# Performance work log

Hardware: AMD Instinct MI355X
Metric: run time of the kernel (lower is better)

## Reference

```python
import jax, jax.numpy as jnp
import numpy as np

N_NODES = 100000
N_EDGES = 1200000
N_GRAPHS = 2048
NUM_SHAPE, NUM_COLOR, NUM_CLASS = 8, 8, 10
MAX_POS, EMB, HID = 20, 16, 64
IN_DIM = 3 * EMB  # 48


def setup_inputs() -> dict:
    key = jax.random.key(0)
    ks = jax.random.split(key, 14)
    x = jax.random.randint(ks[0], (N_NODES, 3), 0, NUM_SHAPE)
    edge_index = jax.random.randint(ks[1], (2, N_EDGES), 0, N_NODES)
    batch = jnp.sort(jax.random.randint(ks[2], (N_NODES,), 0, N_GRAPHS))
    s = 0.1
    return {
        'x': x, 'edge_index': edge_index, 'batch': batch, 'num_graphs': N_GRAPHS,
        'shape_emb': jax.random.normal(ks[3], (NUM_SHAPE, EMB)) * s,
        'color_emb': jax.random.normal(ks[4], (NUM_COLOR, EMB)) * s,
        'pos_emb': jax.random.normal(ks[5], (MAX_POS, EMB)) * s,
        'W1_l': jax.random.normal(ks[6], (IN_DIM, HID)) * s,
        'W1_r': jax.random.normal(ks[7], (IN_DIM, HID)) * s,
        'b1': jnp.zeros((HID,)),
        'W2_l': jax.random.normal(ks[8], (HID, HID)) * s,
        'W2_r': jax.random.normal(ks[9], (HID, HID)) * s,
        'b2': jnp.zeros((HID,)),
        'Wc': jax.random.normal(ks[10], (HID, NUM_CLASS)) * s,
        'bc': jnp.zeros((NUM_CLASS,)),
    }


def _sage(h, src, dst, W_l, W_r, b, n_nodes):
    # mean-aggregate neighbor features x[src] into dst, then linear combine with root
    agg = jax.ops.segment_sum(h[src], dst, num_segments=n_nodes)
    deg = jax.ops.segment_sum(jnp.ones((src.shape[0],), h.dtype), dst, num_segments=n_nodes)
    mean = agg / jnp.maximum(deg, 1.0)[:, None]
    return mean @ W_l + h @ W_r + b


def reference(x, edge_index, batch, num_graphs, shape_emb, color_emb, pos_emb,
              W1_l, W1_r, b1, W2_l, W2_r, b2, Wc, bc):
    n_nodes = x.shape[0]
    shp = shape_emb[x[:, 0]]
    col = color_emb[x[:, 1]]
    pos = pos_emb[jnp.clip(x[:, 2], 0, MAX_POS - 1)]
    h = jnp.concatenate([shp, col, pos], axis=-1)  # [N, 48]
    src, dst = edge_index[0], edge_index[1]
    h = jax.nn.relu(_sage(h, src, dst, W1_l, W1_r, b1, n_nodes))
    h = jax.nn.relu(_sage(h, src, dst, W2_l, W2_r, b2, n_nodes))
    # global mean pool per graph
    gsum = jax.ops.segment_sum(h, batch, num_segments=num_graphs)
    gcnt = jax.ops.segment_sum(jnp.ones((n_nodes,), h.dtype), batch, num_segments=num_graphs)
    hg = gsum / jnp.maximum(gcnt, 1.0)[:, None]
    return hg @ Wc + bc
```

## Files before the change

kernel.cpp:

```cpp
#include <hip/hip_runtime.h>

#define N_NODES 100000
#define N_EDGES 1200000
#define N_GRAPHS 2048
#define CAPA 16
#define CAPB 32
#define NBUCK 500
#define DPB 200
#define BCAP 4864
#define TILE 4096

typedef unsigned int uint;
typedef unsigned short ushort;
typedef __attribute__((ext_vector_type(8))) short short8;
typedef __attribute__((ext_vector_type(4))) float f32x4;

__device__ __forceinline__ int atomAddI(int* p, int v) {
    return __hip_atomic_fetch_add(p, v, __ATOMIC_RELAXED, __HIP_MEMORY_SCOPE_AGENT);
}
__device__ __forceinline__ int clampPos(int v) { return min(max(v, 0), 19); }
__device__ __forceinline__ uint f2bf(float f) {
    uint b = __float_as_uint(f);
    return (b + 0x7fffu + ((b >> 16) & 1u)) >> 16;
}
__device__ __forceinline__ int bucketOf(int d) {
    return (int)(((uint)((d >> 3) * 5243)) >> 17);
}

__global__ __launch_bounds__(256) void k_init(
    const int* __restrict__ x,
    const float* __restrict__ se, const float* __restrict__ ce,
    const float* __restrict__ pe,
    const float* __restrict__ W1l, const float* __restrict__ W1r,
    const float* __restrict__ b1,
    const float* __restrict__ W2l, const float* __restrict__ W2r,
    ushort* __restrict__ WLt, ushort* __restrict__ WstkT,
    int* __restrict__ gcur, int* __restrict__ xpk) {
    int t = blockIdx.x * 256 + threadIdx.x;
    if (t < 64 * 96) {
        int col = t / 96, k = t - (t / 96) * 96;
        float v = 0.f;
        if (k < 72) {
            int bkt = (k < 36) ? k : (k - 36);
            const float* erow; int f0;
            if (bkt < 8)       { erow = se + bkt * 16;        f0 = 0;  }
            else if (bkt < 16) { erow = ce + (bkt - 8) * 16;  f0 = 16; }
            else               { erow = pe + (bkt - 16) * 16; f0 = 32; }
            const float* W = (k < 36) ? W1l : W1r;
            float a = 0.f;
            #pragma unroll
            for (int f = 0; f < 16; ++f) a = fmaf(erow[f], W[(f0 + f) * 64 + col], a);
            v = a;
        } else if (k == 72) {
            v = b1[col];
        }
        WLt[t] = (ushort)f2bf(v);
    }
    if (t < 64 * 128) {
        int col = t >> 7, k = t & 127;
        float wv = (k < 64) ? W2r[k * 64 + col] : W2l[(k - 64) * 64 + col];
        WstkT[col * 128 + k] = (ushort)f2bf(wv);
    }
    if (t < NBUCK) gcur[t] = 0;
    for (int i = t; i < N_NODES; i += 256 * 256) {
        int xs = x[i * 3 + 0], xc = x[i * 3 + 1], xp = clampPos(x[i * 3 + 2]);
        xpk[i] = xs | (xc << 8) | (xp << 16);
    }
}

__global__ __launch_bounds__(256) void k_bin(const int* __restrict__ ei,
                                             int* __restrict__ gcur,
                                             int2* __restrict__ binned) {
    __shared__ int hist[NBUCK], offs[NBUCK], runc[NBUCK], gbase[NBUCK];
    __shared__ int2 stag[TILE];
    int tid = threadIdx.x;
    int tile_base = blockIdx.x * TILE;
    int tile_n = min(TILE, N_EDGES - tile_base);
    int n4 = tile_n >> 2;
    const int4* s4p = (const int4*)(ei + tile_base);
    const int4* d4p = (const int4*)(ei + N_EDGES + tile_base);

    for (int t = tid; t < NBUCK; t += 256) hist[t] = 0;
    __syncthreads();
    for (int k = tid; k < n4; k += 256) {
        int4 d4 = d4p[k];
        #pragma unroll
        for (int i = 0; i < 4; ++i) atomicAdd(&hist[bucketOf((&d4.x)[i])], 1);
    }
    __syncthreads();
    if (tid < 64) {
        int carry = 0;
        for (int c = 0; c < 8; ++c) {
            int idx = c * 64 + tid;
            int v = (idx < NBUCK) ? hist[idx] : 0;
            int orig = v;
            #pragma unroll
            for (int o = 1; o < 64; o <<= 1) {
                int u = __shfl_up(v, o);
                if (tid >= o) v += u;
            }
            if (idx < NBUCK) offs[idx] = carry + v - orig;
            carry += __shfl(v, 63);
        }
    }
    __syncthreads();
    for (int t = tid; t < NBUCK; t += 256) runc[t] = offs[t];
    __syncthreads();
    for (int k = tid; k < n4; k += 256) {
        int4 d4 = d4p[k];
        int4 s4 = s4p[k];
        #pragma unroll
        for (int i = 0; i < 4; ++i) {
            int b = bucketOf((&d4.x)[i]);
            int pos = atomicAdd(&runc[b], 1);
            stag[pos] = make_int2((&s4.x)[i], (&d4.x)[i]);
        }
    }
    __syncthreads();
    for (int t = tid; t < NBUCK; t += 256) gbase[t] = atomAddI(&gcur[t], hist[t]);
    __syncthreads();
    for (int i = tid; i < tile_n; i += 256) {
        int2 p = stag[i];
        int b = bucketOf(p.y);
        int o = gbase[b] + (i - offs[b]);
        if (o < BCAP) binned[(size_t)b * BCAP + o] = p;
    }
}

__global__ __launch_bounds__(256) void k_place(const int2* __restrict__ binned,
                                               const int* __restrict__ gcur,
                                               int* __restrict__ cursor,
                                               int* __restrict__ slabA,
                                               int* __restrict__ slabB) {
    __shared__ int lslab[DPB][CAPA + CAPB];
    __shared__ int lcur[DPB];
    int b = blockIdx.x;
    int tid = threadIdx.x;
    if (tid < DPB) lcur[tid] = 0;
    __syncthreads();
    int n = min(gcur[b], BCAP);
    const int2* in = binned + (size_t)b * BCAP;
    for (int i = tid; i < n; i += 256) {
        int2 p = in[i];
        int local = p.y - b * DPB;
        int slot = atomicAdd(&lcur[local], 1);
        if (slot < CAPA + CAPB) lslab[local][slot] = p.x;
    }
    __syncthreads();
    for (int i = tid; i < DPB * CAPA; i += 256)
        slabA[b * DPB * CAPA + i] = lslab[i >> 4][i & 15];
    for (int i = tid; i < DPB * CAPB; i += 256)
        slabB[b * DPB * CAPB + i] = lslab[i >> 5][CAPA + (i & 31)];
    if (tid < DPB) cursor[b * DPB + tid] = lcur[tid];
}

__device__ __forceinline__ int slabAt(const int* __restrict__ slabA,
                                      const int* __restrict__ slabB,
                                      int row, int idx) {
    return (idx < CAPA) ? slabA[row * CAPA + idx] : slabB[row * CAPB + idx - CAPA];
}

__global__ __launch_bounds__(256) void k_layer1(
    const int* __restrict__ xpk, const int* __restrict__ cursor,
    const int* __restrict__ slabA, const int* __restrict__ slabB,
    const ushort* __restrict__ WLt, uint* __restrict__ AbU) {
    __shared__ int    cnt[16][104];
    __shared__ ushort scnt[16][104];
    __shared__ float  sinv[16];
    __shared__ int    sdeg[16];
    int tid = threadIdx.x;
    int row0 = blockIdx.x * 16;
    for (int i = tid; i < 16 * 104; i += 256) cnt[i / 104][i % 104] = 0;
    if (tid < 16) {
        int dg = cursor[row0 + tid];
        sdeg[tid] = min(dg, CAPA + CAPB);
        sinv[tid] = 1.0f / fmaxf((float)dg, 1.0f);
    }
    __syncthreads();
    for (int i = tid; i < 16 * 48; i += 256) {
        int r = i / 48, idx = i - r * 48;
        if (idx < sdeg[r]) {
            int p = xpk[slabAt(slabA, slabB, row0 + r, idx)];
            atomicAdd(&cnt[r][p & 0xff], 1);
            atomicAdd(&cnt[r][8 + ((p >> 8) & 0xff)], 1);
            atomicAdd(&cnt[r][16 + (p >> 16)], 1);
        }
    }
    if (tid < 16) {
        int p0 = xpk[row0 + tid];
        cnt[tid][36 + (p0 & 0xff)] = 1;
        cnt[tid][44 + ((p0 >> 8) & 0xff)] = 1;
        cnt[tid][52 + (p0 >> 16)] = 1;
        cnt[tid][72] = 1;
    }
    __syncthreads();
    for (int i = tid; i < 16 * 96; i += 256) {
        int r = i / 96, k = i - r * 96;
        float v = (float)cnt[r][k];
        if (k < 36) v *= sinv[r];
        scnt[r][k] = (ushort)f2bf(v);
    }
    __syncthreads();
    int w = tid >> 6, lane = tid & 63;
    int lo16 = lane & 15, hi4 = lane >> 4;
    f32x4 acc = {0.f, 0.f, 0.f, 0.f};
    #pragma unroll
    for (int ks = 0; ks < 3; ++ks) {
        short8 a8 = *(const short8*)(&scnt[lo16][ks * 32 + hi4 * 8]);
        short8 b8 = *(const short8*)(WLt + (w * 16 + lo16) * 96 + ks * 32 + hi4 * 8);
        acc = __builtin_amdgcn_mfma_f32_16x16x32_bf16(a8, b8, acc, 0, 0, 0);
    }
    #pragma unroll
    for (int r = 0; r < 4; ++r) {
        uint rb = f2bf(fmaxf(acc[r], 0.0f));
        uint nxt = __shfl_down(rb, 1);
        if ((lo16 & 1) == 0) {
            int node = row0 + hi4 * 4 + r;
            AbU[(size_t)node * 64 + ((w * 16 + lo16) >> 1)] = rb | (nxt << 16);
        }
    }
}

__global__ __launch_bounds__(256) void k_gather(
    uint* __restrict__ AbU, const int* __restrict__ cursor,
    const int* __restrict__ slabA, const int* __restrict__ slabB) {
    int gid = blockIdx.x * 256 + threadIdx.x;
    int wid = gid >> 6;
    int lane = threadIdx.x & 63;
    int half = lane >> 5, l = lane & 31;
    int row = wid * 2 + half;
    if (row >= N_NODES) return;
    int deg = cursor[row];
    int m = min(deg, CAPA + CAPB);
    int nb0 = (l < m)      ? slabAt(slabA, slabB, row, l)      : 0;
    int nb1 = (l + 32 < m) ? slabB[row * CAPB + l + 32 - CAPA] : 0;
    float ax = 0.f, ay = 0.f;
    int d = 0;
    for (; d + 2 <= m; d += 2) {
        int s0 = __shfl((d < 32) ? nb0 : nb1, (half << 5) | (d & 31));
        int s1 = __shfl((d + 1 < 32) ? nb0 : nb1, (half << 5) | ((d + 1) & 31));
        uint v0 = AbU[(size_t)s0 * 64 + l];
        uint v1 = AbU[(size_t)s1 * 64 + l];
        ax += __uint_as_float(v0 << 16) + __uint_as_float(v1 << 16);
        ay += __uint_as_float(v0 & 0xffff0000u) + __uint_as_float(v1 & 0xffff0000u);
    }
    if (d < m) {
        int s = __shfl((d < 32) ? nb0 : nb1, (half << 5) | (d & 31));
        uint v = AbU[(size_t)s * 64 + l];
        ax += __uint_as_float(v << 16);
        ay += __uint_as_float(v & 0xffff0000u);
    }
    float inv = 1.0f / fmaxf((float)deg, 1.0f);
    AbU[(size_t)row * 64 + 32 + l] = f2bf(ax * inv) | (f2bf(ay * inv) << 16);
}

__global__ __launch_bounds__(256) void k_gemm(
    const uint* __restrict__ AbU, const ushort* __restrict__ WstkT,
    const float* __restrict__ b2, float* __restrict__ h2) {
    int w = threadIdx.x >> 6, lane = threadIdx.x & 63;
    int lo16 = lane & 15, hi4 = lane >> 4;
    short8 bfr[4][4];
    #pragma unroll
    for (int nb = 0; nb < 4; ++nb) {
        #pragma unroll
        for (int kb = 0; kb < 4; ++kb)
            bfr[nb][kb] = *(const short8*)(WstkT + (nb * 16 + lo16) * 128 + kb * 32 + hi4 * 8);
    }
    float bb[4];
    #pragma unroll
    for (int nb = 0; nb < 4; ++nb) bb[nb] = b2[nb * 16 + lo16];

    int row0 = blockIdx.x * 64 + w * 16;
    int arow = min(row0 + lo16, N_NODES - 1);
    const short8* Arow = (const short8*)(AbU + (size_t)arow * 64);
    short8 a8[4];
    #pragma unroll
    for (int kb = 0; kb < 4; ++kb) a8[kb] = Arow[kb * 4 + hi4];

    f32x4 acc[4] = {{0,0,0,0},{0,0,0,0},{0,0,0,0},{0,0,0,0}};
    #pragma unroll
    for (int kb = 0; kb < 4; ++kb) {
        #pragma unroll
        for (int nb = 0; nb < 4; ++nb)
            acc[nb] = __builtin_amdgcn_mfma_f32_16x16x32_bf16(a8[kb], bfr[nb][kb], acc[nb], 0, 0, 0);
    }
    #pragma unroll
    for (int nb = 0; nb < 4; ++nb) {
        #pragma unroll
        for (int r = 0; r < 4; ++r) {
            int orow = row0 + hi4 * 4 + r;
            if (orow < N_NODES)
                h2[(size_t)orow * 64 + nb * 16 + lo16] = fmaxf(acc[nb][r] + bb[nb], 0.f);
        }
    }
}

__device__ __forceinline__ int lowerBound(const int* __restrict__ b, int n, int v) {
    int lo = 0, hi = n;
    while (lo < hi) { int mid = (lo + hi) >> 1; if (b[mid] < v) lo = mid + 1; else hi = mid; }
    return lo;
}

__global__ __launch_bounds__(256) void k_pool_final(
    const float* __restrict__ h2, const int* __restrict__ batch,
    const float* __restrict__ Wc, const float* __restrict__ bc,
    float* __restrict__ out) {
    int g = blockIdx.x * 4 + (threadIdx.x >> 6);
    if (g >= N_GRAPHS) return;
    int j = threadIdx.x & 63;
    int lo = lowerBound(batch, N_NODES, g);
    int hi = lowerBound(batch, N_NODES, g + 1);
    float a0 = 0.f, a1 = 0.f, a2 = 0.f, a3 = 0.f;
    int n = lo;
    for (; n + 4 <= hi; n += 4) {
        a0 += h2[(size_t)n * 64 + j];
        a1 += h2[(size_t)(n + 1) * 64 + j];
        a2 += h2[(size_t)(n + 2) * 64 + j];
        a3 += h2[(size_t)(n + 3) * 64 + j];
    }
    for (; n < hi; ++n) a0 += h2[(size_t)n * 64 + j];
    float mean = ((a0 + a1) + (a2 + a3)) / fmaxf((float)(hi - lo), 1.0f);
    #pragma unroll
    for (int c = 0; c < 10; ++c) {
        float p = mean * Wc[j * 10 + c];
        #pragma unroll
        for (int off = 32; off >= 1; off >>= 1) p += __shfl_down(p, off);
        if (j == 0) out[g * 10 + c] = p + bc[c];
    }
}

extern "C" void kernel_launch(void* const* d_in, const int* in_sizes, int n_in,
                              void* d_out, int out_size, void* d_ws, size_t ws_size,
                              hipStream_t stream) {
    const int* x     = (const int*)d_in[0];
    const int* ei    = (const int*)d_in[1];
    const int* batch = (const int*)d_in[2];
    const float* se  = (const float*)d_in[4];
    const float* ce  = (const float*)d_in[5];
    const float* pe  = (const float*)d_in[6];
    const float* W1l = (const float*)d_in[7];
    const float* W1r = (const float*)d_in[8];
    const float* b1  = (const float*)d_in[9];
    const float* W2l = (const float*)d_in[10];
    const float* W2r = (const float*)d_in[11];
    const float* b2  = (const float*)d_in[12];
    const float* Wc  = (const float*)d_in[13];
    const float* bc  = (const float*)d_in[14];

    float* ws    = (float*)d_ws;
    uint*  AbU   = (uint*)ws;
    float* h2    = ws + 6400000;
    int2*  binned= (int2*)ws;
    int*   slabA = (int*)(ws + 12800000);
    int*   slabB = (int*)(ws + 14400000);
    int*   cursor= (int*)(ws + 17600000);
    int*   xpk   = (int*)(ws + 17700000);
    ushort* WstkT= (ushort*)(ws + 17806000);
    ushort* WLt  = (ushort*)(ws + 17810100);
    int*   gcur  = (int*)(ws + 17814000);

    k_init<<<256, 256, 0, stream>>>(x, se, ce, pe, W1l, W1r, b1, W2l, W2r,
                                    WLt, WstkT, gcur, xpk);
    k_bin<<<(N_EDGES + TILE - 1) / TILE, 256, 0, stream>>>(ei, gcur, binned);
    k_place<<<NBUCK, 256, 0, stream>>>(binned, gcur, cursor, slabA, slabB);
    k_layer1<<<N_NODES / 16, 256, 0, stream>>>(xpk, cursor, slabA, slabB, WLt, AbU);
    k_gather<<<12500, 256, 0, stream>>>(AbU, cursor, slabA, slabB);
    k_gemm<<<(N_NODES + 63) / 64, 256, 0, stream>>>(AbU, WstkT, b2, h2);
    k_pool_final<<<(N_GRAPHS + 3) / 4, 256, 0, stream>>>(h2, batch, Wc, bc, (float*)d_out);
}
```

Baseline: 128.9 us.

## Fuse layer-2 gather with GEMM via LDS and store h2 as bf16

Merges the neighbour-mean gather and the layer-2 GEMM into one kernel. Each block builds its 64-row tile of [root | mean] features in shared memory and runs the MFMA GEMM from there, so the mean no longer goes to global memory and one launch is dropped. The layer-2 output is now stored as packed bf16 instead of fp32, which halves the traffic into the pooling kernel; pooling uses 32-lane groups over bf16 pairs. The cost is lower output precision, and the fused kernel now does its gather work over fewer waves per row, which could hurt latency hiding.

```diff
diff --git a/kernel.cpp b/kernel.cpp
--- a/kernel.cpp
+++ b/kernel.cpp
@@ -23,6 +23,8 @@
     uint b = __float_as_uint(f);
     return (b + 0x7fffu + ((b >> 16) & 1u)) >> 16;
 }
+__device__ __forceinline__ float bfLo(uint v) { return __uint_as_float(v << 16); }
+__device__ __forceinline__ float bfHi(uint v) { return __uint_as_float(v & 0xffff0000u); }
 __device__ __forceinline__ int bucketOf(int d) {
     return (int)(((uint)((d >> 3) * 5243)) >> 17);
 }
@@ -221,43 +223,47 @@
     }
 }
 
-__global__ __launch_bounds__(256) void k_gather(
-    uint* __restrict__ AbU, const int* __restrict__ cursor,
-    const int* __restrict__ slabA, const int* __restrict__ slabB) {
-    int gid = blockIdx.x * 256 + threadIdx.x;
-    int wid = gid >> 6;
-    int lane = threadIdx.x & 63;
+__global__ __launch_bounds__(256) void k_g2(
+    const uint* __restrict__ AbU, const int* __restrict__ cursor,
+    const int* __restrict__ slabA, const int* __restrict__ slabB,
+    const ushort* __restrict__ WstkT, const float* __restrict__ b2,
+    uint* __restrict__ h2b) {
+    __shared__ uint Ab[64][68];
+    int tid = threadIdx.x;
+    int row0 = blockIdx.x * 64;
+    for (int i = tid; i < 64 * 32; i += 256) {
+        int r = i >> 5, c = i & 31;
+        int gr = min(row0 + r, N_NODES - 1);
+        Ab[r][c] = AbU[(size_t)gr * 64 + c];
+    }
+    int w = tid >> 6, lane = tid & 63;
     int half = lane >> 5, l = lane & 31;
-    int row = wid * 2 + half;
-    if (row >= N_NODES) return;
-    int deg = cursor[row];
-    int m = min(deg, CAPA + CAPB);
-    int nb0 = (l < m)      ? slabAt(slabA, slabB, row, l)      : 0;
-    int nb1 = (l + 32 < m) ? slabB[row * CAPB + l + 32 - CAPA] : 0;
-    float ax = 0.f, ay = 0.f;
-    int d = 0;
-    for (; d + 2 <= m; d += 2) {
-        int s0 = __shfl((d < 32) ? nb0 : nb1, (half << 5) | (d & 31));
-        int s1 = __shfl((d + 1 < 32) ? nb0 : nb1, (half << 5) | ((d + 1) & 31));
-        uint v0 = AbU[(size_t)s0 * 64 + l];
-        uint v1 = AbU[(size_t)s1 * 64 + l];
-        ax += __uint_as_float(v0 << 16) + __uint_as_float(v1 << 16);
-        ay += __uint_as_float(v0 & 0xffff0000u) + __uint_as_float(v1 & 0xffff0000u);
-    }
-    if (d < m) {
-        int s = __shfl((d < 32) ? nb0 : nb1, (half << 5) | (d & 31));
-        uint v = AbU[(size_t)s * 64 + l];
-        ax += __uint_as_float(v << 16);
-        ay += __uint_as_float(v & 0xffff0000u);
-    }
-    float inv = 1.0f / fmaxf((float)deg, 1.0f);
-    AbU[(size_t)row * 64 + 32 + l] = f2bf(ax * inv) | (f2bf(ay * inv) << 16);
-}
-
-__global__ __launch_bounds__(256) void k_gemm(
-    const uint* __restrict__ AbU, const ushort* __restrict__ WstkT,
-    const float* __restrict__ b2, float* __restrict__ h2) {
-    int w = threadIdx.x >> 6, lane = threadIdx.x & 63;
+    for (int pr = 0; pr < 8; ++pr) {
+        int lr = w * 16 + pr * 2 + half;
+        int row = row0 + lr;
+        int deg = 0, m = 0;
+        if (row < N_NODES) { deg = cursor[row]; m = min(deg, CAPA + CAPB); }
+        int nb0 = (l < m)      ? slabAt(slabA, slabB, row, l)      : 0;
+        int nb1 = (l + 32 < m) ? slabB[row * CAPB + l + 32 - CAPA] : 0;
+        float ax = 0.f, ay = 0.f;
+        int d = 0;
+        for (; d + 2 <= m; d += 2) {
+            int s0 = __shfl((d < 32) ? nb0 : nb1, (half << 5) | (d & 31));
+            int s1 = __shfl((d + 1 < 32) ? nb0 : nb1, (half << 5) | ((d + 1) & 31));
+            uint v0 = AbU[(size_t)s0 * 64 + l];
+            uint v1 = AbU[(size_t)s1 * 64 + l];
+            ax += bfLo(v0) + bfLo(v1);
+            ay += bfHi(v0) + bfHi(v1);
+        }
+        if (d < m) {
+            int s = __shfl((d < 32) ? nb0 : nb1, (half << 5) | (d & 31));
+            uint v = AbU[(size_t)s * 64 + l];
+            ax += bfLo(v);
+            ay += bfHi(v);
+        }
+        float inv = 1.0f / fmaxf((float)deg, 1.0f);
+        Ab[lr][32 + l] = f2bf(ax * inv) | (f2bf(ay * inv) << 16);
+    }
     int lo16 = lane & 15, hi4 = lane >> 4;
     short8 bfr[4][4];
     #pragma unroll
@@ -269,14 +275,11 @@
     float bb[4];
     #pragma unroll
     for (int nb = 0; nb < 4; ++nb) bb[nb] = b2[nb * 16 + lo16];
-
-    int row0 = blockIdx.x * 64 + w * 16;
-    int arow = min(row0 + lo16, N_NODES - 1);
-    const short8* Arow = (const short8*)(AbU + (size_t)arow * 64);
+    __syncthreads();
     short8 a8[4];
     #pragma unroll
-    for (int kb = 0; kb < 4; ++kb) a8[kb] = Arow[kb * 4 + hi4];
-
+    for (int kb = 0; kb < 4; ++kb)
+        a8[kb] = *(const short8*)(&Ab[w * 16 + lo16][kb * 16 + hi4 * 4]);
     f32x4 acc[4] = {{0,0,0,0},{0,0,0,0},{0,0,0,0},{0,0,0,0}};
     #pragma unroll
     for (int kb = 0; kb < 4; ++kb) {
@@ -288,9 +291,13 @@
     for (int nb = 0; nb < 4; ++nb) {
         #pragma unroll
         for (int r = 0; r < 4; ++r) {
-            int orow = row0 + hi4 * 4 + r;
-            if (orow < N_NODES)
-                h2[(size_t)orow * 64 + nb * 16 + lo16] = fmaxf(acc[nb][r] + bb[nb], 0.f);
+            uint rb = f2bf(fmaxf(acc[nb][r] + bb[nb], 0.0f));
+            uint nxt = __shfl_down(rb, 1);
+            if ((lo16 & 1) == 0) {
+                int orow = row0 + w * 16 + hi4 * 4 + r;
+                if (orow < N_NODES)
+                    h2b[(size_t)orow * 32 + ((nb * 16 + lo16) >> 1)] = rb | (nxt << 16);
+            }
         }
     }
 }
@@ -302,30 +309,34 @@
 }
 
 __global__ __launch_bounds__(256) void k_pool_final(
-    const float* __restrict__ h2, const int* __restrict__ batch,
+    const uint* __restrict__ h2b, const int* __restrict__ batch,
     const float* __restrict__ Wc, const float* __restrict__ bc,
     float* __restrict__ out) {
-    int g = blockIdx.x * 4 + (threadIdx.x >> 6);
+    int g = blockIdx.x * 8 + (threadIdx.x >> 5);
     if (g >= N_GRAPHS) return;
-    int j = threadIdx.x & 63;
+    int l = threadIdx.x & 31;
     int lo = lowerBound(batch, N_NODES, g);
     int hi = lowerBound(batch, N_NODES, g + 1);
-    float a0 = 0.f, a1 = 0.f, a2 = 0.f, a3 = 0.f;
+    float ax0 = 0.f, ay0 = 0.f, ax1 = 0.f, ay1 = 0.f;
     int n = lo;
-    for (; n + 4 <= hi; n += 4) {
-        a0 += h2[(size_t)n * 64 + j];
-        a1 += h2[(size_t)(n + 1) * 64 + j];
-        a2 += h2[(size_t)(n + 2) * 64 + j];
-        a3 += h2[(size_t)(n + 3) * 64 + j];
-    }
-    for (; n < hi; ++n) a0 += h2[(size_t)n * 64 + j];
-    float mean = ((a0 + a1) + (a2 + a3)) / fmaxf((float)(hi - lo), 1.0f);
+    for (; n + 2 <= hi; n += 2) {
+        uint v0 = h2b[(size_t)n * 32 + l];
+        uint v1 = h2b[(size_t)(n + 1) * 32 + l];
+        ax0 += bfLo(v0); ay0 += bfHi(v0);
+        ax1 += bfLo(v1); ay1 += bfHi(v1);
+    }
+    if (n < hi) {
+        uint v = h2b[(size_t)n * 32 + l];
+        ax0 += bfLo(v); ay0 += bfHi(v);
+    }
+    float inv = 1.0f / fmaxf((float)(hi - lo), 1.0f);
+    float mx = (ax0 + ax1) * inv, my = (ay0 + ay1) * inv;
     #pragma unroll
     for (int c = 0; c < 10; ++c) {
-        float p = mean * Wc[j * 10 + c];
-        #pragma unroll
-        for (int off = 32; off >= 1; off >>= 1) p += __shfl_down(p, off);
-        if (j == 0) out[g * 10 + c] = p + bc[c];
+        float p = fmaf(mx, Wc[(2 * l) * 10 + c], my * Wc[(2 * l + 1) * 10 + c]);
+        #pragma unroll
+        for (int off = 16; off >= 1; off >>= 1) p += __shfl_xor(p, off);
+        if (l == 0) out[g * 10 + c] = p + bc[c];
     }
 }
 
@@ -349,7 +360,7 @@
 
     float* ws    = (float*)d_ws;
     uint*  AbU   = (uint*)ws;
-    float* h2    = ws + 6400000;
+    uint*  h2b   = (uint*)(ws + 6400000);
     int2*  binned= (int2*)ws;
     int*   slabA = (int*)(ws + 12800000);
     int*   slabB = (int*)(ws + 14400000);
@@ -364,7 +375,7 @@
     k_bin<<<(N_EDGES + TILE - 1) / TILE, 256, 0, stream>>>(ei, gcur, binned);
     k_place<<<NBUCK, 256, 0, stream>>>(binned, gcur, cursor, slabA, slabB);
     k_layer1<<<N_NODES / 16, 256, 0, stream>>>(xpk, cursor, slabA, slabB, WLt, AbU);
-    k_gather<<<12500, 256, 0, stream>>>(AbU, cursor, slabA, slabB);
-    k_gemm<<<(N_NODES + 63) / 64, 256, 0, stream>>>(AbU, WstkT, b2, h2);
-    k_pool_final<<<(N_GRAPHS + 3) / 4, 256, 0, stream>>>(h2, batch, Wc, bc, (float*)d_out);
-}
+    k_g2<<<(N_NODES + 63) / 64, 256, 0, stream>>>(AbU, cursor, slabA, slabB,
+                                                  WstkT, b2, h2b);
+    k_pool_final<<<N_GRAPHS / 8, 256, 0, stream>>>(h2b, batch, Wc, bc, (float*)d_out);
+}
```

Result: slower. 154.8 us (+20.1%).
